# Performance work log

Measured on AMD Instinct MI355X. Metric: run time of the kernel, lower is better.

Reference implementation:

```python
import jax, jax.numpy as jnp
import numpy as np

B_, H, N, D = 512, 8, 256, 16   # windows*batch, heads, tokens/window, head_dim
NW = 64                          # windows per image (B_ = 8 images * 64 windows)
TABLE = 961                      # (2*16-1)^2 relative position table rows
EPS = 1e-12                      # F.normalize eps


def setup_inputs() -> dict:
    key = jax.random.key(0)
    k_q, k_k, k_v, k_t, k_i, k_m = jax.random.split(key, 6)
    return {
        "q": jax.random.normal(k_q, (B_, H, N, D), dtype=jnp.float32),
        "k": jax.random.normal(k_k, (B_, H, N, D), dtype=jnp.float32),
        "v": jax.random.normal(k_v, (B_, H, N, D), dtype=jnp.float32),
        "table": jax.random.normal(k_t, (TABLE, H), dtype=jnp.float32),
        "index": jax.random.randint(k_i, (N * N,), 0, TABLE, dtype=jnp.int64),
        "mask": jax.random.normal(k_m, (NW, N, N), dtype=jnp.float32),
    }


def _l2norm(x):
    # matches F.normalize(x, dim=-1): x / max(||x||2, eps)
    n = jnp.sqrt(jnp.sum(x * x, axis=-1, keepdims=True))
    return x / jnp.maximum(n, EPS)


def reference(q, k, v, table, index, mask):
    b, h, n, d = q.shape
    # cosine-normalized QK^T: [B_, H, N, N]
    attn = jnp.einsum("bhnd,bhmd->bhnm", _l2norm(q), _l2norm(k))
    # relative position bias gather: table[index] -> (N*N, H) -> (H, N, N)
    bias = table[index].reshape(n, n, h).transpose(2, 0, 1)
    attn = attn + bias[None]
    # per-window additive mask
    nw = mask.shape[0]
    attn = attn.reshape(b // nw, nw, h, n, n) + mask[None, :, None]
    attn = attn.reshape(b, h, n, n)
    attn = jax.nn.softmax(attn, axis=-1)   # attn_drop is identity at p=0
    x = jnp.einsum("bhnm,bhmd->bhnd", attn, v)
    # transpose(1,2).reshape(B_, N, H*head_dim)
    return x.transpose(0, 2, 1, 3).reshape(b, n, h * d)
```

## Files before the change

kernel.cpp:

```cpp
#include <hip/hip_runtime.h>
#include <stdint.h>

#define HH 8
#define NN 256
#define DD 16
#define NWIN 64
#define LOG2E 1.44269504088896340736f

typedef __attribute__((ext_vector_type(8))) short short8;
typedef __attribute__((ext_vector_type(4))) short short4_t;
typedef __attribute__((ext_vector_type(4))) float f32x4;

static __device__ __forceinline__ unsigned short f2bf(float f) {
    union { float f; uint32_t u; } v; v.f = f;
    uint32_t u = v.u;
    uint32_t r = (u + 0x7fffu + ((u >> 16) & 1u)) >> 16;
    return (unsigned short)r;
}
static __device__ __forceinline__ float bf2f(uint32_t s) {
    union { uint32_t u; float f; } v; v.u = s << 16;
    return v.f;
}

__global__ void bias_perm_kernel(const float* __restrict__ table,
                                 const int* __restrict__ index,
                                 unsigned short* __restrict__ biasD) {
    int o = blockIdx.x * 256 + threadIdx.x;
    int r  = o & 3;
    int c  = (o >> 2) & 15;
    int qq = (o >> 6) & 3;
    int jt = (o >> 8) & 15;
    int it = (o >> 12) & 15;
    int h  = o >> 16;
    int i = it * 16 + c;
    int j = jt * 16 + qq * 4 + r;
    int idx = index[i * NN + j];
    biasD[o] = f2bf(table[idx * HH + h] * LOG2E);
}

__global__ void mask_perm_kernel(const float* __restrict__ mask,
                                 unsigned short* __restrict__ maskD) {
    __shared__ float lds[16 * 256];
    int w  = blockIdx.x >> 4;
    int it = blockIdx.x & 15;
    int tid = threadIdx.x;
    const float* src = mask + ((size_t)w * NN + it * 16) * NN;
    {
        int row = tid >> 4, col0 = (tid & 15) * 16;
        const float4* s4 = (const float4*)(src + row * NN + col0);
        float4* d4 = (float4*)(lds + row * 256 + col0);
        d4[0] = s4[0]; d4[1] = s4[1]; d4[2] = s4[2]; d4[3] = s4[3];
    }
    __syncthreads();
    unsigned short* dst = maskD + (size_t)blockIdx.x * 4096 + tid * 16;
    int base = tid * 16;
#pragma unroll
    for (int e = 0; e < 16; e++) {
        int o  = base + e;
        int r  = o & 3;
        int c  = (o >> 2) & 15;
        int qq = (o >> 6) & 3;
        int jt = (o >> 8) & 15;
        int j  = jt * 16 + qq * 4 + r;
        dst[e] = f2bf(lds[c * 256 + j] * LOG2E);
    }
}

__global__ __launch_bounds__(256, 2) void attn_kernel(
    const float* __restrict__ q, const float* __restrict__ k, const float* __restrict__ v,
    const unsigned short* __restrict__ biasD, const unsigned short* __restrict__ maskD,
    float* __restrict__ out)
{
    int bh = blockIdx.x;
    int b  = bh >> 3;
    int h  = bh & 7;
    int w  = b & (NWIN - 1);
    int tid  = threadIdx.x;
    int lane = tid & 63;
    int wave = tid >> 6;
    int c    = lane & 15;
    int quad = lane >> 4;

    __shared__ unsigned short Kn[256 * 20];
    __shared__ unsigned short Vl[4096];
    __shared__ float Xs[256 * 17];

    const size_t base = (size_t)bh * (NN * DD);

    {
        const float4* kr = (const float4*)(k + base + (size_t)tid * DD);
        float4 a0 = kr[0], a1 = kr[1], a2 = kr[2], a3 = kr[3];
        float x[16] = {a0.x,a0.y,a0.z,a0.w, a1.x,a1.y,a1.z,a1.w,
                       a2.x,a2.y,a2.z,a2.w, a3.x,a3.y,a3.z,a3.w};
        float ss = 0.f;
#pragma unroll
        for (int e = 0; e < 16; e++) ss += x[e] * x[e];
        float sc = 1.0f / fmaxf(sqrtf(ss), 1e-12f);
        unsigned short* dst = &Kn[tid * 20];
#pragma unroll
        for (int e = 0; e < 16; e++) dst[e] = f2bf(x[e] * sc);
    }
    {
        const float4* vr = (const float4*)(v + base + (size_t)tid * DD);
        float4 a0 = vr[0], a1 = vr[1], a2 = vr[2], a3 = vr[3];
        float x[16] = {a0.x,a0.y,a0.z,a0.w, a1.x,a1.y,a1.z,a1.w,
                       a2.x,a2.y,a2.z,a2.w, a3.x,a3.y,a3.z,a3.w};
        int j  = tid;
        int kc = j >> 5, hi = (j >> 4) & 1, qv = (j >> 2) & 3, r = j & 3;
        int jj = hi * 4 + r;
#pragma unroll
        for (int d = 0; d < 16; d++)
            Vl[((kc * 4 + qv) * 16 + d) * 8 + jj] = f2bf(x[d]);
    }
    __syncthreads();

    short8 vf[8];
#pragma unroll
    for (int kc = 0; kc < 8; kc++)
        vf[kc] = *(const short8*)&Vl[((kc * 4 + quad) * 16 + c) * 8];

    f32x4 zero = {0.f, 0.f, 0.f, 0.f};

#pragma unroll 1
    for (int t = 0; t < 4; t++) {
        int it = wave * 4 + t;
        int i0 = it * 16;

        short8 qf = {0,0,0,0,0,0,0,0};
        if (quad < 2) {
            const float4* qr = (const float4*)(q + base + (size_t)(i0 + c) * DD + quad * 8);
            float4 a0 = qr[0], a1 = qr[1];
            float x[8] = {a0.x,a0.y,a0.z,a0.w, a1.x,a1.y,a1.z,a1.w};
            float ss = 0.f;
#pragma unroll
            for (int e = 0; e < 8; e++) ss += x[e] * x[e];
            ss += __shfl_xor(ss, 16);
            float sc = LOG2E / fmaxf(sqrtf(ss), 1e-12f);
#pragma unroll
            for (int e = 0; e < 8; e++) qf[e] = (short)f2bf(x[e] * sc);
        }

        f32x4 acc[16];
#pragma unroll
        for (int jt = 0; jt < 16; jt++) {
            short8 kf = {0,0,0,0,0,0,0,0};
            if (quad < 2) {
                const unsigned short* kp = &Kn[(jt * 16 + c) * 20 + quad * 8];
                short4_t lo = *(const short4_t*)kp;
                short4_t hi = *(const short4_t*)(kp + 4);
                kf[0]=lo[0]; kf[1]=lo[1]; kf[2]=lo[2]; kf[3]=lo[3];
                kf[4]=hi[0]; kf[5]=hi[1]; kf[6]=hi[2]; kf[7]=hi[3];
            }
            acc[jt] = __builtin_amdgcn_mfma_f32_16x16x32_bf16(kf, qf, zero, 0, 0, 0);
        }

        const unsigned short* bD = biasD + (size_t)(h * 16 + it) * 4096 + quad * 64 + c * 4;
        const unsigned short* mD = maskD + (size_t)(w * 16 + it) * 4096 + quad * 64 + c * 4;
        float mx = -1e30f;
#pragma unroll
        for (int jt = 0; jt < 16; jt++) {
            uint2 bu = *(const uint2*)(bD + jt * 256);
            uint2 mu = *(const uint2*)(mD + jt * 256);
            acc[jt][0] += bf2f(bu.x & 0xffffu) + bf2f(mu.x & 0xffffu);
            acc[jt][1] += bf2f(bu.x >> 16)     + bf2f(mu.x >> 16);
            acc[jt][2] += bf2f(bu.y & 0xffffu) + bf2f(mu.y & 0xffffu);
            acc[jt][3] += bf2f(bu.y >> 16)     + bf2f(mu.y >> 16);
            mx = fmaxf(mx, fmaxf(fmaxf(acc[jt][0], acc[jt][1]),
                                 fmaxf(acc[jt][2], acc[jt][3])));
        }
        mx = fmaxf(mx, __shfl_xor(mx, 16));
        mx = fmaxf(mx, __shfl_xor(mx, 32));
        float sum = 0.f;
#pragma unroll
        for (int jt = 0; jt < 16; jt++) {
#pragma unroll
            for (int r = 0; r < 4; r++) {
                float e = __builtin_amdgcn_exp2f(acc[jt][r] - mx);
                acc[jt][r] = e;
                sum += e;
            }
        }
        sum += __shfl_xor(sum, 16);
        sum += __shfl_xor(sum, 32);
        float rs = __builtin_amdgcn_rcpf(sum);

        f32x4 xacc = {0.f, 0.f, 0.f, 0.f};
#pragma unroll
        for (int kc = 0; kc < 8; kc++) {
            short8 pf;
#pragma unroll
            for (int hi = 0; hi < 2; hi++) {
                int jt = kc * 2 + hi;
#pragma unroll
                for (int r = 0; r < 4; r++)
                    pf[hi * 4 + r] = (short)f2bf(acc[jt][r] * rs);
            }
            xacc = __builtin_amdgcn_mfma_f32_16x16x32_bf16(vf[kc], pf, xacc, 0, 0, 0);
        }

#pragma unroll
        for (int r = 0; r < 4; r++)
            Xs[(i0 + c) * 17 + quad * 4 + r] = xacc[r];
    }
    __syncthreads();

#pragma unroll
    for (int rep = 0; rep < 4; rep++) {
        int i    = rep * 64 + (tid >> 2);
        int part = tid & 3;
        float4 val;
        val.x = Xs[i * 17 + part * 4 + 0];
        val.y = Xs[i * 17 + part * 4 + 1];
        val.z = Xs[i * 17 + part * 4 + 2];
        val.w = Xs[i * 17 + part * 4 + 3];
        float4* dst = (float4*)(out + ((size_t)b * NN + i) * (HH * DD) + h * DD + part * 4);
        *dst = val;
    }
}

extern "C" void kernel_launch(void* const* d_in, const int* in_sizes, int n_in,
                              void* d_out, int out_size, void* d_ws, size_t ws_size,
                              hipStream_t stream) {
    const float* q     = (const float*)d_in[0];
    const float* k     = (const float*)d_in[1];
    const float* v     = (const float*)d_in[2];
    const float* table = (const float*)d_in[3];
    const int*   index = (const int*)d_in[4];
    const float* mask  = (const float*)d_in[5];
    float* out = (float*)d_out;

    unsigned short* biasD = (unsigned short*)d_ws;
    unsigned short* maskD = biasD + (size_t)HH * NN * NN;

    bias_perm_kernel<<<2048, 256, 0, stream>>>(table, index, biasD);
    mask_perm_kernel<<<1024, 256, 0, stream>>>(mask, maskD);
    attn_kernel<<<4096, 256, 0, stream>>>(q, k, v, biasD, maskD, out);
}
```

Baseline: 389.9 us.

## Fold bias+mask into MFMA accumulator init, defer softmax scaling, drop LDS output staging

Bias and mask are now permuted so each lane loads 16-byte chunks, and they are summed directly into the MFMA C operand instead of being added after the QK product. K is stored pre-swizzled and zero-padded lanes are replaced by duplicated K loads, so the quad<2 branch disappears. Softmax normalization is applied once to the PV output rather than to every probability, and PV uses two independent accumulators. The Xs LDS staging and final barrier are removed in favour of direct float4 stores, and launch bounds are raised to 4 blocks/SM. The mask permute kernel becomes a simple one-element-per-thread gather without LDS.

```diff
diff --git a/kernel.cpp b/kernel.cpp
--- a/kernel.cpp
+++ b/kernel.cpp
@@ -8,65 +8,59 @@
 #define LOG2E 1.44269504088896340736f
 
 typedef __attribute__((ext_vector_type(8))) short short8;
-typedef __attribute__((ext_vector_type(4))) short short4_t;
 typedef __attribute__((ext_vector_type(4))) float f32x4;
 
 static __device__ __forceinline__ unsigned short f2bf(float f) {
-    union { float f; uint32_t u; } v; v.f = f;
-    uint32_t u = v.u;
-    uint32_t r = (u + 0x7fffu + ((u >> 16) & 1u)) >> 16;
-    return (unsigned short)r;
-}
-static __device__ __forceinline__ float bf2f(uint32_t s) {
-    union { uint32_t u; float f; } v; v.u = s << 16;
-    return v.f;
+    uint32_t u = __builtin_bit_cast(uint32_t, f);
+    return (unsigned short)((u + 0x7fffu + ((u >> 16) & 1u)) >> 16);
+}
+static __device__ __forceinline__ uint32_t rne(uint32_t u) {
+    return u + 0x7fffu + ((u >> 16) & 1u);
+}
+static __device__ __forceinline__ uint32_t pk2bf(float a, float b) {
+    uint32_t ua = __builtin_bit_cast(uint32_t, a);
+    uint32_t ub = __builtin_bit_cast(uint32_t, b);
+    return (rne(ua) >> 16) | (rne(ub) & 0xffff0000u);
+}
+static __device__ __forceinline__ float blo(uint32_t u) {
+    return __builtin_bit_cast(float, u << 16);
+}
+static __device__ __forceinline__ float bhi(uint32_t u) {
+    return __builtin_bit_cast(float, u & 0xffff0000u);
 }
 
 __global__ void bias_perm_kernel(const float* __restrict__ table,
                                  const int* __restrict__ index,
                                  unsigned short* __restrict__ biasD) {
     int o = blockIdx.x * 256 + threadIdx.x;
-    int r  = o & 3;
-    int c  = (o >> 2) & 15;
-    int qq = (o >> 6) & 3;
-    int jt = (o >> 8) & 15;
-    int it = (o >> 12) & 15;
-    int h  = o >> 16;
-    int i = it * 16 + c;
-    int j = jt * 16 + qq * 4 + r;
-    int idx = index[i * NN + j];
-    biasD[o] = f2bf(table[idx * HH + h] * LOG2E);
+    int r   = o & 3;
+    int jtl = (o >> 2) & 1;
+    int cc  = (o >> 3) & 15;
+    int qq  = (o >> 7) & 3;
+    int jth = (o >> 9) & 7;
+    int it  = (o >> 12) & 15;
+    int h   = o >> 16;
+    int i = it * 16 + cc;
+    int j = (jth * 2 + jtl) * 16 + qq * 4 + r;
+    biasD[o] = f2bf(table[index[i * NN + j] * HH + h] * LOG2E);
 }
 
 __global__ void mask_perm_kernel(const float* __restrict__ mask,
                                  unsigned short* __restrict__ maskD) {
-    __shared__ float lds[16 * 256];
-    int w  = blockIdx.x >> 4;
-    int it = blockIdx.x & 15;
-    int tid = threadIdx.x;
-    const float* src = mask + ((size_t)w * NN + it * 16) * NN;
-    {
-        int row = tid >> 4, col0 = (tid & 15) * 16;
-        const float4* s4 = (const float4*)(src + row * NN + col0);
-        float4* d4 = (float4*)(lds + row * 256 + col0);
-        d4[0] = s4[0]; d4[1] = s4[1]; d4[2] = s4[2]; d4[3] = s4[3];
-    }
-    __syncthreads();
-    unsigned short* dst = maskD + (size_t)blockIdx.x * 4096 + tid * 16;
-    int base = tid * 16;
-#pragma unroll
-    for (int e = 0; e < 16; e++) {
-        int o  = base + e;
-        int r  = o & 3;
-        int c  = (o >> 2) & 15;
-        int qq = (o >> 6) & 3;
-        int jt = (o >> 8) & 15;
-        int j  = jt * 16 + qq * 4 + r;
-        dst[e] = f2bf(lds[c * 256 + j] * LOG2E);
-    }
-}
-
-__global__ __launch_bounds__(256, 2) void attn_kernel(
+    int o = blockIdx.x * 256 + threadIdx.x;
+    int r   = o & 3;
+    int jtl = (o >> 2) & 1;
+    int cc  = (o >> 3) & 15;
+    int qq  = (o >> 7) & 3;
+    int jth = (o >> 9) & 7;
+    int it  = (o >> 12) & 15;
+    int w   = o >> 16;
+    int i = it * 16 + cc;
+    int j = (jth * 2 + jtl) * 16 + qq * 4 + r;
+    maskD[o] = f2bf(mask[((size_t)w * NN + i) * NN + j] * LOG2E);
+}
+
+__global__ __launch_bounds__(256, 4) void attn_kernel(
     const float* __restrict__ q, const float* __restrict__ k, const float* __restrict__ v,
     const unsigned short* __restrict__ biasD, const unsigned short* __restrict__ maskD,
     float* __restrict__ out)
@@ -81,13 +75,13 @@
     int c    = lane & 15;
     int quad = lane >> 4;
 
-    __shared__ unsigned short Kn[256 * 20];
-    __shared__ unsigned short Vl[4096];
-    __shared__ float Xs[256 * 17];
+    __shared__ __align__(16) unsigned short Kf[256 * 16];
+    __shared__ __align__(16) unsigned short Vl[4096];
 
     const size_t base = (size_t)bh * (NN * DD);
 
     {
+        int jt = tid >> 4, cc = tid & 15;
         const float4* kr = (const float4*)(k + base + (size_t)tid * DD);
         float4 a0 = kr[0], a1 = kr[1], a2 = kr[2], a3 = kr[3];
         float x[16] = {a0.x,a0.y,a0.z,a0.w, a1.x,a1.y,a1.z,a1.w,
@@ -96,9 +90,13 @@
 #pragma unroll
         for (int e = 0; e < 16; e++) ss += x[e] * x[e];
         float sc = 1.0f / fmaxf(sqrtf(ss), 1e-12f);
-        unsigned short* dst = &Kn[tid * 20];
-#pragma unroll
-        for (int e = 0; e < 16; e++) dst[e] = f2bf(x[e] * sc);
+        uint32_t p[8];
+#pragma unroll
+        for (int e = 0; e < 8; e++) p[e] = pk2bf(x[2*e] * sc, x[2*e+1] * sc);
+        uint4 w0 = {p[0], p[1], p[2], p[3]};
+        uint4 w1 = {p[4], p[5], p[6], p[7]};
+        *(uint4*)&Kf[((jt * 2 + 0) * 16 + cc) * 8] = w0;
+        *(uint4*)&Kf[((jt * 2 + 1) * 16 + cc) * 8] = w1;
     }
     {
         const float4* vr = (const float4*)(v + base + (size_t)tid * DD);
@@ -114,11 +112,7 @@
     }
     __syncthreads();
 
-    short8 vf[8];
-#pragma unroll
-    for (int kc = 0; kc < 8; kc++)
-        vf[kc] = *(const short8*)&Vl[((kc * 4 + quad) * 16 + c) * 8];
-
+    const unsigned short* Kbase = &Kf[((quad & 1) * 16 + c) * 8];
     f32x4 zero = {0.f, 0.f, 0.f, 0.f};
 
 #pragma unroll 1
@@ -136,35 +130,33 @@
             for (int e = 0; e < 8; e++) ss += x[e] * x[e];
             ss += __shfl_xor(ss, 16);
             float sc = LOG2E / fmaxf(sqrtf(ss), 1e-12f);
-#pragma unroll
-            for (int e = 0; e < 8; e++) qf[e] = (short)f2bf(x[e] * sc);
-        }
-
+            union { short8 s; uint32_t u[4]; } pq;
+#pragma unroll
+            for (int e = 0; e < 4; e++) pq.u[e] = pk2bf(x[2*e] * sc, x[2*e+1] * sc);
+            qf = pq.s;
+        }
+
+        const unsigned short* bB = biasD + ((h * 16 + it) * 4096 + quad * 128 + c * 8);
+        const unsigned short* mB = maskD + ((w * 16 + it) * 4096 + quad * 128 + c * 8);
         f32x4 acc[16];
 #pragma unroll
+        for (int jth = 0; jth < 8; jth++) {
+            uint4 bu = *(const uint4*)(bB + jth * 512);
+            uint4 mu = *(const uint4*)(mB + jth * 512);
+            f32x4 c0, c1;
+            c0[0] = blo(bu.x) + blo(mu.x); c0[1] = bhi(bu.x) + bhi(mu.x);
+            c0[2] = blo(bu.y) + blo(mu.y); c0[3] = bhi(bu.y) + bhi(mu.y);
+            c1[0] = blo(bu.z) + blo(mu.z); c1[1] = bhi(bu.z) + bhi(mu.z);
+            c1[2] = blo(bu.w) + blo(mu.w); c1[3] = bhi(bu.w) + bhi(mu.w);
+            short8 kf0 = *(const short8*)(Kbase + (jth * 2 + 0) * 256);
+            short8 kf1 = *(const short8*)(Kbase + (jth * 2 + 1) * 256);
+            acc[jth * 2 + 0] = __builtin_amdgcn_mfma_f32_16x16x32_bf16(kf0, qf, c0, 0, 0, 0);
+            acc[jth * 2 + 1] = __builtin_amdgcn_mfma_f32_16x16x32_bf16(kf1, qf, c1, 0, 0, 0);
+        }
+
+        float mx = -1e30f;
+#pragma unroll
         for (int jt = 0; jt < 16; jt++) {
-            short8 kf = {0,0,0,0,0,0,0,0};
-            if (quad < 2) {
-                const unsigned short* kp = &Kn[(jt * 16 + c) * 20 + quad * 8];
-                short4_t lo = *(const short4_t*)kp;
-                short4_t hi = *(const short4_t*)(kp + 4);
-                kf[0]=lo[0]; kf[1]=lo[1]; kf[2]=lo[2]; kf[3]=lo[3];
-                kf[4]=hi[0]; kf[5]=hi[1]; kf[6]=hi[2]; kf[7]=hi[3];
-            }
-            acc[jt] = __builtin_amdgcn_mfma_f32_16x16x32_bf16(kf, qf, zero, 0, 0, 0);
-        }
-
-        const unsigned short* bD = biasD + (size_t)(h * 16 + it) * 4096 + quad * 64 + c * 4;
-        const unsigned short* mD = maskD + (size_t)(w * 16 + it) * 4096 + quad * 64 + c * 4;
-        float mx = -1e30f;
-#pragma unroll
-        for (int jt = 0; jt < 16; jt++) {
-            uint2 bu = *(const uint2*)(bD + jt * 256);
-            uint2 mu = *(const uint2*)(mD + jt * 256);
-            acc[jt][0] += bf2f(bu.x & 0xffffu) + bf2f(mu.x & 0xffffu);
-            acc[jt][1] += bf2f(bu.x >> 16)     + bf2f(mu.x >> 16);
-            acc[jt][2] += bf2f(bu.y & 0xffffu) + bf2f(mu.y & 0xffffu);
-            acc[jt][3] += bf2f(bu.y >> 16)     + bf2f(mu.y >> 16);
             mx = fmaxf(mx, fmaxf(fmaxf(acc[jt][0], acc[jt][1]),
                                  fmaxf(acc[jt][2], acc[jt][3])));
         }
@@ -184,36 +176,32 @@
         sum += __shfl_xor(sum, 32);
         float rs = __builtin_amdgcn_rcpf(sum);
 
-        f32x4 xacc = {0.f, 0.f, 0.f, 0.f};
-#pragma unroll
-        for (int kc = 0; kc < 8; kc++) {
-            short8 pf;
+        f32x4 xa = zero, xb = zero;
+#pragma unroll
+        for (int kc = 0; kc < 8; kc += 2) {
+            short8 vfa = *(const short8*)&Vl[((kc * 4 + quad) * 16 + c) * 8];
+            short8 vfb = *(const short8*)&Vl[(((kc + 1) * 4 + quad) * 16 + c) * 8];
+            union { short8 s; uint32_t u[4]; } pa, pb;
 #pragma unroll
             for (int hi = 0; hi < 2; hi++) {
                 int jt = kc * 2 + hi;
-#pragma unroll
-                for (int r = 0; r < 4; r++)
-                    pf[hi * 4 + r] = (short)f2bf(acc[jt][r] * rs);
+                pa.u[hi * 2 + 0] = pk2bf(acc[jt][0], acc[jt][1]);
+                pa.u[hi * 2 + 1] = pk2bf(acc[jt][2], acc[jt][3]);
+                int ju = (kc + 1) * 2 + hi;
+                pb.u[hi * 2 + 0] = pk2bf(acc[ju][0], acc[ju][1]);
+                pb.u[hi * 2 + 1] = pk2bf(acc[ju][2], acc[ju][3]);
             }
-            xacc = __builtin_amdgcn_mfma_f32_16x16x32_bf16(vf[kc], pf, xacc, 0, 0, 0);
-        }
-
-#pragma unroll
-        for (int r = 0; r < 4; r++)
-            Xs[(i0 + c) * 17 + quad * 4 + r] = xacc[r];
-    }
-    __syncthreads();
-
-#pragma unroll
-    for (int rep = 0; rep < 4; rep++) {
-        int i    = rep * 64 + (tid >> 2);
-        int part = tid & 3;
+            xa = __builtin_amdgcn_mfma_f32_16x16x32_bf16(vfa, pa.s, xa, 0, 0, 0);
+            xb = __builtin_amdgcn_mfma_f32_16x16x32_bf16(vfb, pb.s, xb, 0, 0, 0);
+        }
+
         float4 val;
-        val.x = Xs[i * 17 + part * 4 + 0];
-        val.y = Xs[i * 17 + part * 4 + 1];
-        val.z = Xs[i * 17 + part * 4 + 2];
-        val.w = Xs[i * 17 + part * 4 + 3];
-        float4* dst = (float4*)(out + ((size_t)b * NN + i) * (HH * DD) + h * DD + part * 4);
+        val.x = (xa[0] + xb[0]) * rs;
+        val.y = (xa[1] + xb[1]) * rs;
+        val.z = (xa[2] + xb[2]) * rs;
+        val.w = (xa[3] + xb[3]) * rs;
+        float4* dst = (float4*)(out + ((size_t)(b * NN + i0 + c)) * (HH * DD)
+                                + h * DD + quad * 4);
         *dst = val;
     }
 }
@@ -233,6 +221,6 @@
     unsigned short* maskD = biasD + (size_t)HH * NN * NN;
 
     bias_perm_kernel<<<2048, 256, 0, stream>>>(table, index, biasD);
-    mask_perm_kernel<<<1024, 256, 0, stream>>>(mask, maskD);
+    mask_perm_kernel<<<16384, 256, 0, stream>>>(mask, maskD);
     attn_kernel<<<4096, 256, 0, stream>>>(q, k, v, biasD, maskD, out);
 }
```

After: 490.7 us. 1.26x slower.
